# Optimization experiments

Hardware: AMD Instinct MI355X
Metric: run time of the kernel (lower is better)

The kernel has to match this reference:

```python
import jax, jax.numpy as jnp
import numpy as np

HIDDEN_DIM = 640
VOCAB_SIZE = 1024


def setup_inputs() -> dict:
    key = jax.random.key(0)
    kf, kp, kw, kb = jax.random.split(key, 4)
    B, T, U, H, V = 8, 256, 64, HIDDEN_DIM, VOCAB_SIZE
    f = jax.random.normal(kf, (B, T, H), dtype=jnp.float32)
    p = jax.random.normal(kp, (B, U, H), dtype=jnp.float32)
    # nn.Linear default init: U(-1/sqrt(H), 1/sqrt(H))
    bound = 1.0 / np.sqrt(H)
    W = jax.random.uniform(kw, (V, H), minval=-bound, maxval=bound, dtype=jnp.float32)
    b = jax.random.uniform(kb, (V,), minval=-bound, maxval=bound, dtype=jnp.float32)
    return {"f": f, "p": p, "W": W, "b": b}


def reference(f, p, W, b):
    # f: (B,T,H), p: (B,U,H) -> combined: (B,T,U,H)
    combined = f[:, :, None, :] + p[:, None, :, :]
    h = jax.nn.relu(combined)
    # Linear: h @ W^T + b -> (B,T,U,V)
    logits = jnp.einsum('btuh,vh->btuv', h, W) + b
    return logits
```

## Files before the change

kernel.cpp:

```cpp
#include <hip/hip_runtime.h>
#include <hip/hip_bf16.h>

#define BDIM 8
#define TDIM 256
#define UDIM 64
#define HDIM 640
#define VDIM 1024
#define MDIM (BDIM * TDIM * UDIM)

#define BK 32
#define NT (HDIM / BK)
#define NKC (HDIM / 8)

typedef __attribute__((ext_vector_type(8))) short short8;
typedef __attribute__((ext_vector_type(4))) float f32x4;

__device__ __forceinline__ ushort f2bf(float x) {
    union { float f; unsigned int u; } v; v.f = x;
    unsigned int r = (v.u + 0x7fffu + ((v.u >> 16) & 1u)) >> 16;
    return (ushort)r;
}


__global__ __launch_bounds__(256) void cvt_w_tiled_kernel(
    const float* __restrict__ W, ushort* __restrict__ Wt)
{
    const int c  = blockIdx.x * 256 + threadIdx.x;
    const int lr = c & 15;
    const int q  = c >> 4;
    const int kc = q % NKC;
    const int g  = q / NKC;
    const int v  = g * 16 + lr;
    const float* src = W + (size_t)v * HDIM + kc * 8;
    f32x4 w0 = *(const f32x4*)src;
    f32x4 w1 = *(const f32x4*)(src + 4);
    short8 o;
    #pragma unroll
    for (int e = 0; e < 4; ++e) {
        o[e]     = (short)f2bf(w0[e]);
        o[e + 4] = (short)f2bf(w1[e]);
    }
    *(short8*)(Wt + (size_t)c * 8) = o;
}

__global__ __launch_bounds__(256) void build_h_tiled_kernel(
    const float* __restrict__ f, const float* __restrict__ p,
    ushort* __restrict__ ht)
{
    const int c  = blockIdx.x * 256 + threadIdx.x;
    const int lr = c & 15;
    const int q  = c >> 4;
    const int kc = q % NKC;
    const int g  = q / NKC;
    const int m  = g * 16 + lr;
    const int b  = m >> 14;
    const int t  = (m >> 6) & (TDIM - 1);
    const int u  = m & (UDIM - 1);
    const int k  = kc * 8;
    const float* fr = f + (size_t)(b * TDIM + t) * HDIM + k;
    const float* pr = p + (size_t)(b * UDIM + u) * HDIM + k;
    f32x4 f0 = *(const f32x4*)fr;
    f32x4 f1 = *(const f32x4*)(fr + 4);
    f32x4 p0 = *(const f32x4*)pr;
    f32x4 p1 = *(const f32x4*)(pr + 4);
    short8 o;
    #pragma unroll
    for (int e = 0; e < 4; ++e) {
        float a0 = fmaxf(f0[e] + p0[e], 0.0f);
        float a1 = fmaxf(f1[e] + p1[e], 0.0f);
        o[e]     = (short)f2bf(a0);
        o[e + 4] = (short)f2bf(a1);
    }
    *(short8*)(ht + (size_t)c * 8) = o;
}

__global__ __launch_bounds__(256, 2) void hgemm_regT_kernel(
    const ushort* __restrict__ ht,
    const ushort* __restrict__ Wt,
    const float* __restrict__ bias,
    float* __restrict__ out)
{
    const int tid  = threadIdx.x;
    const int lane = tid & 63;
    const int wave = tid >> 6;
    const int wm   = wave >> 1;
    const int wn   = wave & 1;

    const int bid   = blockIdx.x;
    const int work  = (bid & 7) * 512 + (bid >> 3);
    const int mtile = work >> 3;
    const int ntile = work & 7;
    const int m0 = mtile * 256;
    const int v0 = ntile * 128;

    const int gA = mtile * 16 + wm * 8;
    const int gB = ntile * 8 + wn * 4;
    const int la = lane * 8;

    int abase[8], bbase[4];
    #pragma unroll
    for (int mi = 0; mi < 8; ++mi) abase[mi] = (gA + mi) * (NKC * 128) + la;
    #pragma unroll
    for (int ni = 0; ni < 4; ++ni) bbase[ni] = (gB + ni) * (NKC * 128) + la;

    f32x4 acc[8][4];
    #pragma unroll
    for (int i = 0; i < 8; ++i)
        #pragma unroll
        for (int j = 0; j < 4; ++j)
            acc[i][j] = (f32x4)0.0f;

    short8 a0[8], b0[4], a1[8], b1[4];

#define LOADF(A, B, kt) do {                                                   \
        const int ko_ = (kt) * 512;                                            \
        _Pragma("unroll")                                                      \
        for (int i_ = 0; i_ < 8; ++i_)                                         \
            (A)[i_] = *(const short8*)(ht + abase[i_] + ko_);                  \
        _Pragma("unroll")                                                      \
        for (int i_ = 0; i_ < 4; ++i_)                                         \
            (B)[i_] = *(const short8*)(Wt + bbase[i_] + ko_);                  \
    } while (0)

#define MFMAS(A, B) do {                                                       \
        __builtin_amdgcn_s_setprio(1);                                         \
        _Pragma("unroll")                                                      \
        for (int mi_ = 0; mi_ < 8; ++mi_)                                      \
            _Pragma("unroll")                                                  \
            for (int ni_ = 0; ni_ < 4; ++ni_)                                  \
                acc[mi_][ni_] = __builtin_amdgcn_mfma_f32_16x16x32_bf16(       \
                    (A)[mi_], (B)[ni_], acc[mi_][ni_], 0, 0, 0);               \
        __builtin_amdgcn_s_setprio(0);                                         \
    } while (0)

    LOADF(a0, b0, 0);
    #pragma unroll 1
    for (int t = 0; t < NT; t += 2) {
        LOADF(a1, b1, t + 1);
        MFMAS(a0, b0);
        if (t + 2 < NT) LOADF(a0, b0, t + 2);
        MFMAS(a1, b1);
    }
#undef LOADF
#undef MFMAS

    const int lr = lane & 15;
    #pragma unroll
    for (int ni = 0; ni < 4; ++ni) {
        const int col = v0 + wn * 64 + ni * 16 + lr;
        const float bv = bias[col];
        #pragma unroll
        for (int mi = 0; mi < 8; ++mi) {
            const int rbase = m0 + wm * 128 + mi * 16 + ((lane >> 4) << 2);
            #pragma unroll
            for (int reg = 0; reg < 4; ++reg) {
                out[(size_t)(rbase + reg) * VDIM + col] = acc[mi][ni][reg] + bv;
            }
        }
    }
}

__global__ void cvt_w_kernel(const float* __restrict__ W, ushort* __restrict__ Wb) {
    int i = (blockIdx.x * 256 + threadIdx.x) * 4;
    f32x4 w = *(const f32x4*)(W + i);
    ushort4 o;
    o.x = f2bf(w[0]); o.y = f2bf(w[1]); o.z = f2bf(w[2]); o.w = f2bf(w[3]);
    *(ushort4*)(Wb + i) = o;
}

#define GLDS(srcptr, ldsptr)                                                   \
    __builtin_amdgcn_global_load_lds(                                          \
        (const __attribute__((address_space(1))) void*)(srcptr),               \
        (__attribute__((address_space(3))) void*)(ldsptr), 16, 0, 0)

template <bool USE_WB>
__global__ __launch_bounds__(256) void joint_gemm_kernel(
    const float* __restrict__ f, const float* __restrict__ p,
    const float* __restrict__ Wf, const ushort* __restrict__ Wb,
    const float* __restrict__ bias, float* __restrict__ out)
{
    __shared__ ushort Alds[128 * 64];
    __shared__ ushort Blds[128 * 64];

    const int tid  = threadIdx.x;
    const int lane = tid & 63;
    const int wave = tid >> 6;
    const int wm   = wave >> 1;
    const int wn   = wave & 1;

    const int bid   = blockIdx.x;
    const int work  = (bid & 7) * 1024 + (bid >> 3);
    const int mtile = work >> 3;
    const int ntile = work & 7;
    const int m0 = mtile * 128;
    const int v0 = ntile * 128;

    const int b  = m0 >> 14;
    const int t0 = (m0 >> 6) & (TDIM - 1);

    const float*  fbase = f + (size_t)(b * TDIM + t0) * HDIM;
    const float*  pbase = p + (size_t)b * UDIM * HDIM;
    const ushort* wbbase = Wb + (size_t)v0 * HDIM;
    const float*  wfbase = Wf + (size_t)v0 * HDIM;

    f32x4 acc[4][4];
    #pragma unroll
    for (int i = 0; i < 4; ++i)
        #pragma unroll
        for (int j = 0; j < 4; ++j)
            acc[i][j] = (f32x4)0.0f;

    for (int kt = 0; kt < HDIM / 64; ++kt) {
        const int k0 = kt * 64;
        __syncthreads();

        if (USE_WB) {
            #pragma unroll
            for (int it = 0; it < 4; ++it) {
                const int c   = it * 256 + tid;
                const int row = c >> 3;
                const int j   = c & 7;
                const ushort* src = wbbase + row * HDIM + k0 + ((j ^ (row & 7)) << 3);
                GLDS(src, &Blds[(it * 256 + wave * 64) * 8]);
            }
        } else {
            #pragma unroll
            for (int it = 0; it < 4; ++it) {
                const int c   = it * 256 + tid;
                const int row = c >> 3;
                const int j   = c & 7;
                const float* wp = wfbase + row * HDIM + k0 + j * 8;
                f32x4 w0 = *(const f32x4*)wp;
                f32x4 w1 = *(const f32x4*)(wp + 4);
                short8 wv;
                #pragma unroll
                for (int e = 0; e < 4; ++e) {
                    wv[e]     = (short)f2bf(w0[e]);
                    wv[e + 4] = (short)f2bf(w1[e]);
                }
                *(short8*)(&Blds[(row * 8 + (j ^ (row & 7))) * 8]) = wv;
            }
        }

        #pragma unroll
        for (int it = 0; it < 4; ++it) {
            const int c   = it * 256 + tid;
            const int row = c >> 3;
            const int j   = c & 7;
            const float* fp_ = fbase + (row >> 6) * HDIM + k0 + j * 8;
            const float* pp_ = pbase + (row & 63) * HDIM + k0 + j * 8;
            f32x4 f0 = *(const f32x4*)fp_;
            f32x4 f1 = *(const f32x4*)(fp_ + 4);
            f32x4 p0 = *(const f32x4*)pp_;
            f32x4 p1 = *(const f32x4*)(pp_ + 4);
            short8 hv;
            #pragma unroll
            for (int e = 0; e < 4; ++e) {
                float a0 = fmaxf(f0[e] + p0[e], 0.0f);
                float a1 = fmaxf(f1[e] + p1[e], 0.0f);
                hv[e]     = (short)f2bf(a0);
                hv[e + 4] = (short)f2bf(a1);
            }
            *(short8*)(&Alds[(row * 8 + (j ^ (row & 7))) * 8]) = hv;
        }

        __syncthreads();

        #pragma unroll
        for (int ks = 0; ks < 2; ++ks) {
            short8 afr[4], bfr[4];
            #pragma unroll
            for (int mi = 0; mi < 4; ++mi) {
                const int r = wm * 64 + mi * 16 + (lane & 15);
                const int j = ks * 4 + (lane >> 4);
                afr[mi] = *(const short8*)(&Alds[(r * 8 + (j ^ (r & 7))) * 8]);
            }
            #pragma unroll
            for (int ni = 0; ni < 4; ++ni) {
                const int r = wn * 64 + ni * 16 + (lane & 15);
                const int j = ks * 4 + (lane >> 4);
                bfr[ni] = *(const short8*)(&Blds[(r * 8 + (j ^ (r & 7))) * 8]);
            }
            #pragma unroll
            for (int mi = 0; mi < 4; ++mi)
                #pragma unroll
                for (int ni = 0; ni < 4; ++ni)
                    acc[mi][ni] = __builtin_amdgcn_mfma_f32_16x16x32_bf16(
                        afr[mi], bfr[ni], acc[mi][ni], 0, 0, 0);
        }
    }

    #pragma unroll
    for (int ni = 0; ni < 4; ++ni) {
        const int col = v0 + wn * 64 + ni * 16 + (lane & 15);
        const float bv = bias[col];
        #pragma unroll
        for (int mi = 0; mi < 4; ++mi) {
            const int rbase = m0 + wm * 64 + mi * 16 + ((lane >> 4) << 2);
            #pragma unroll
            for (int reg = 0; reg < 4; ++reg) {
                out[(size_t)(rbase + reg) * VDIM + col] = acc[mi][ni][reg] + bv;
            }
        }
    }
}

extern "C" void kernel_launch(void* const* d_in, const int* in_sizes, int n_in,
                              void* d_out, int out_size, void* d_ws, size_t ws_size,
                              hipStream_t stream) {
    const float* f    = (const float*)d_in[0];
    const float* p    = (const float*)d_in[1];
    const float* W    = (const float*)d_in[2];
    const float* bias = (const float*)d_in[3];
    float* out = (float*)d_out;

    const size_t wb_bytes = (size_t)VDIM * HDIM * sizeof(ushort);
    const size_t h_bytes  = (size_t)MDIM * HDIM * sizeof(ushort);

    if (ws_size >= wb_bytes + h_bytes) {
        ushort* Wt = (ushort*)d_ws;
        ushort* ht = (ushort*)((char*)d_ws + wb_bytes);
        cvt_w_tiled_kernel<<<(VDIM * HDIM / 8) / 256, 256, 0, stream>>>(W, Wt);
        build_h_tiled_kernel<<<(MDIM / 256) * (HDIM / 8) / 8 * 8, 256, 0, stream>>>(f, p, ht);
        const int grid = (MDIM / 256) * (VDIM / 128);
        hgemm_regT_kernel<<<grid, 256, 0, stream>>>(ht, Wt, bias, out);
    } else if (ws_size >= wb_bytes) {
        ushort* Wb = (ushort*)d_ws;
        cvt_w_kernel<<<(VDIM * HDIM) / 1024, 256, 0, stream>>>(W, Wb);
        joint_gemm_kernel<true><<<(MDIM / 128) * (VDIM / 128), 256, 0, stream>>>(
            f, p, W, Wb, bias, out);
    } else {
        joint_gemm_kernel<false><<<(MDIM / 128) * (VDIM / 128), 256, 0, stream>>>(
            f, p, W, nullptr, bias, out);
    }
}
```

Measured before the change: 412.7 us.

## Stage GEMM fragments through double-buffered LDS via global_load_lds shared across waves

Each wave used to load all of its own A and B fragments straight from global memory into registers, so the two waves sharing an A or B row each fetched it separately. Now the block loads each 32-wide k-slab of A (16 fragment rows) and B (8 fragment rows) once into double-buffered shared memory using direct global-to-LDS loads, with six loads per wave. All waves then read their fragments from LDS. The goal is to halve redundant global/L2 traffic and overlap the next slab's load with compute, at the cost of two block barriers per k-step and 48 KB of LDS, which may limit occupancy.

After: 408.4 us. No clear change (-1.1%).

```diff
diff --git a/kernel.cpp b/kernel.cpp
--- a/kernel.cpp
+++ b/kernel.cpp
@@ -11,6 +11,7 @@
 #define BK 32
 #define NT (HDIM / BK)
 #define NKC (HDIM / 8)
+#define GSTRIDE (NKC * 128)
 
 typedef __attribute__((ext_vector_type(8))) short short8;
 typedef __attribute__((ext_vector_type(4))) float f32x4;
@@ -74,12 +75,19 @@
     *(short8*)(ht + (size_t)c * 8) = o;
 }
 
-__global__ __launch_bounds__(256, 2) void hgemm_regT_kernel(
+#define GLDS(srcptr, ldsptr)                                                   \
+    __builtin_amdgcn_global_load_lds(                                          \
+        (const __attribute__((address_space(1))) void*)(srcptr),               \
+        (__attribute__((address_space(3))) void*)(ldsptr), 16, 0, 0)
+
+__global__ __launch_bounds__(256, 2) void hgemm_frag_kernel(
     const ushort* __restrict__ ht,
     const ushort* __restrict__ Wt,
     const float* __restrict__ bias,
     float* __restrict__ out)
 {
+    __shared__ ushort Sh[2][12288];
+
     const int tid  = threadIdx.x;
     const int lane = tid & 63;
     const int wave = tid >> 6;
@@ -93,15 +101,23 @@
     const int m0 = mtile * 256;
     const int v0 = ntile * 128;
 
-    const int gA = mtile * 16 + wm * 8;
-    const int gB = ntile * 8 + wn * 4;
-    const int la = lane * 8;
-
-    int abase[8], bbase[4];
-    #pragma unroll
-    for (int mi = 0; mi < 8; ++mi) abase[mi] = (gA + mi) * (NKC * 128) + la;
-    #pragma unroll
-    for (int ni = 0; ni < 4; ++ni) bbase[ni] = (gB + ni) * (NKC * 128) + la;
+    const int gA0 = mtile * 16;
+    const int gB0 = ntile * 8;
+    const int la  = lane * 8;
+
+    const ushort* sbase[6];
+    int doff[6];
+    #pragma unroll
+    for (int i = 0; i < 6; ++i) {
+        const int q = wave * 6 + i;
+        if (q < 16) {
+            sbase[i] = ht + (size_t)(gA0 + q) * GSTRIDE + la;
+            doff[i]  = q * 512;
+        } else {
+            sbase[i] = Wt + (size_t)(gB0 + (q - 16)) * GSTRIDE + la;
+            doff[i]  = 8192 + (q - 16) * 512;
+        }
+    }
 
     f32x4 acc[8][4];
     #pragma unroll
@@ -110,39 +126,49 @@
         for (int j = 0; j < 4; ++j)
             acc[i][j] = (f32x4)0.0f;
 
-    short8 a0[8], b0[4], a1[8], b1[4];
-
-#define LOADF(A, B, kt) do {                                                   \
-        const int ko_ = (kt) * 512;                                            \
+#define STG(kt, bf) do {                                                       \
         _Pragma("unroll")                                                      \
-        for (int i_ = 0; i_ < 8; ++i_)                                         \
-            (A)[i_] = *(const short8*)(ht + abase[i_] + ko_);                  \
+        for (int i_ = 0; i_ < 6; ++i_)                                         \
+            GLDS(sbase[i_] + (kt) * 512, &Sh[bf][doff[i_]]);                   \
+    } while (0)
+
+#define TILE(t, d) do {                                                        \
+        if ((t) + 1 < NT) {                                                    \
+            STG((t) + 1, (d) ^ 1);                                             \
+            asm volatile("s_waitcnt vmcnt(6)" ::: "memory");                   \
+        } else {                                                               \
+            asm volatile("s_waitcnt vmcnt(0)" ::: "memory");                   \
+        }                                                                      \
+        __builtin_amdgcn_sched_barrier(0);                                     \
+        __builtin_amdgcn_s_barrier();         \
+        __builtin_amdgcn_sched_barrier(0);                                     \
+        short8 afr[8], bfr[4];                                                 \
         _Pragma("unroll")                                                      \
-        for (int i_ = 0; i_ < 4; ++i_)                                         \
-            (B)[i_] = *(const short8*)(Wt + bbase[i_] + ko_);                  \
-    } while (0)
-
-#define MFMAS(A, B) do {                                                       \
+        for (int mi = 0; mi < 8; ++mi)                                         \
+            afr[mi] = *(const short8*)(&Sh[d][(wm * 8 + mi) * 512 + la]);      \
+        _Pragma("unroll")                                                      \
+        for (int ni = 0; ni < 4; ++ni)                                         \
+            bfr[ni] = *(const short8*)(&Sh[d][8192 + (wn * 4 + ni) * 512 + la]);\
         __builtin_amdgcn_s_setprio(1);                                         \
         _Pragma("unroll")                                                      \
-        for (int mi_ = 0; mi_ < 8; ++mi_)                                      \
+        for (int mi = 0; mi < 8; ++mi)                                         \
             _Pragma("unroll")                                                  \
-            for (int ni_ = 0; ni_ < 4; ++ni_)                                  \
-                acc[mi_][ni_] = __builtin_amdgcn_mfma_f32_16x16x32_bf16(       \
-                    (A)[mi_], (B)[ni_], acc[mi_][ni_], 0, 0, 0);               \
+            for (int ni = 0; ni < 4; ++ni)                                     \
+                acc[mi][ni] = __builtin_amdgcn_mfma_f32_16x16x32_bf16(         \
+                    afr[mi], bfr[ni], acc[mi][ni], 0, 0, 0);                   \
         __builtin_amdgcn_s_setprio(0);                                         \
+        __builtin_amdgcn_sched_barrier(0);                                     \
+        __builtin_amdgcn_s_barrier();              \
     } while (0)
 
-    LOADF(a0, b0, 0);
+    STG(0, 0);
     #pragma unroll 1
     for (int t = 0; t < NT; t += 2) {
-        LOADF(a1, b1, t + 1);
-        MFMAS(a0, b0);
-        if (t + 2 < NT) LOADF(a0, b0, t + 2);
-        MFMAS(a1, b1);
-    }
-#undef LOADF
-#undef MFMAS
+        TILE(t, 0);
+        TILE(t + 1, 1);
+    }
+#undef TILE
+#undef STG
 
     const int lr = lane & 15;
     #pragma unroll
@@ -167,11 +193,6 @@
     o.x = f2bf(w[0]); o.y = f2bf(w[1]); o.z = f2bf(w[2]); o.w = f2bf(w[3]);
     *(ushort4*)(Wb + i) = o;
 }
-
-#define GLDS(srcptr, ldsptr)                                                   \
-    __builtin_amdgcn_global_load_lds(                                          \
-        (const __attribute__((address_space(1))) void*)(srcptr),               \
-        (__attribute__((address_space(3))) void*)(ldsptr), 16, 0, 0)
 
 template <bool USE_WB>
 __global__ __launch_bounds__(256) void joint_gemm_kernel(
@@ -321,9 +342,9 @@
         ushort* Wt = (ushort*)d_ws;
         ushort* ht = (ushort*)((char*)d_ws + wb_bytes);
         cvt_w_tiled_kernel<<<(VDIM * HDIM / 8) / 256, 256, 0, stream>>>(W, Wt);
-        build_h_tiled_kernel<<<(MDIM / 256) * (HDIM / 8) / 8 * 8, 256, 0, stream>>>(f, p, ht);
+        build_h_tiled_kernel<<<(MDIM / 256) * (HDIM / 8), 256, 0, stream>>>(f, p, ht);
         const int grid = (MDIM / 256) * (VDIM / 128);
-        hgemm_regT_kernel<<<grid, 256, 0, stream>>>(ht, Wt, bias, out);
+        hgemm_frag_kernel<<<grid, 256, 0, stream>>>(ht, Wt, bias, out);
     } else if (ws_size >= wb_bytes) {
         ushort* Wb = (ushort*)d_ws;
         cvt_w_kernel<<<(VDIM * HDIM) / 1024, 256, 0, stream>>>(W, Wb);
```
